# Kernel optimization log

Hardware: AMD Instinct MI355X
Metric: run time of the kernel (lower is better)

Reference implementation:

```python
import jax, jax.numpy as jnp
from jax import lax
import numpy as np

BINS = 256

def setup_inputs() -> dict:
    key = jax.random.key(0)
    k1, k2 = jax.random.split(key)
    B, C, H, W = 8, 3, 1024, 1024
    dst = jax.random.uniform(k1, (B, C, H, W), dtype=jnp.float32)
    ref = jax.random.uniform(k2, (B, C, H, W), dtype=jnp.float32)
    return {"dst": dst, "ref": ref}


def _cal_hist(img):
    # img: [B,C,H,W] in [0,1]. torch.histc(img*255, bins=256, min=0, max=255):
    # bin width = 255/256, so bin = floor(img*255 / (255/256)) = floor(img*256).
    # Inputs are in [0,1) so nothing is out of histc's range (clip is a no-op safeguard).
    B, C, H, W = img.shape
    bc = B * C
    x = img.reshape(bc, H * W)
    idx = jnp.clip(jnp.floor(x * float(BINS)).astype(jnp.int32), 0, BINS - 1)
    rows = jnp.arange(bc, dtype=jnp.int32)[:, None]
    counts = jnp.zeros((bc, BINS), jnp.float32).at[rows, idx].add(1.0)
    # F.normalize(p=1, dim=1) with eps=1e-12
    counts = counts / jnp.maximum(jnp.sum(counts, axis=1, keepdims=True), 1e-12)
    # triu-bmm == cumulative sum -> per-channel CDF
    return jnp.cumsum(counts, axis=1)


def _trans_row(cdf_dst, cdf_ref):
    # Faithful vectorization of the sequential two-pointer loop in cal_trans.
    # For each i (pointer j only ever advances): match at the smallest
    # j' >= j with cdf_ref[j'-1] <= d <= cdf_ref[j']; if impossible, j runs
    # off to 256 and this and all later entries become 255.
    def step(j, d):
        s = jnp.searchsorted(cdf_ref, d)            # smallest s with cdf_ref[s] >= d, in [0,256]
        cand = jnp.maximum(j, s)                    # pointer never moves backwards; cand in [1,256]
        ok = (j < BINS) & (cand <= BINS - 1) & (d >= cdf_ref[cand - 1])
        out = jnp.where(ok, cand, BINS - 1)
        j_next = jnp.where(ok, cand, jnp.int32(BINS))
        return j_next, out.astype(jnp.int32)
    _, tail = lax.scan(step, jnp.int32(1), cdf_dst[1:])  # i = 1..255
    table = jnp.concatenate([jnp.zeros(1, jnp.int32), tail])  # table[0] = arange init = 0
    return table.at[BINS - 1].set(BINS - 1)                   # table[:,255] = 255


def reference(dst, ref):
    B, C, H, W = dst.shape
    bc = B * C
    hist_dst = _cal_hist(dst)   # [BC,256] CDFs
    hist_ref = _cal_hist(ref)
    tables = jax.vmap(_trans_row)(hist_dst, hist_ref)  # [BC,256] int32
    # NOTE: original code indexes tables[b*c] (not b*C+c) -- bug preserved faithfully.
    b_idx = jnp.arange(B, dtype=jnp.int32)[:, None]
    c_idx = jnp.arange(C, dtype=jnp.int32)[None, :]
    row_sel = (b_idx * c_idx).reshape(-1)               # [BC]
    luts = tables[row_sel]                              # [BC,256]
    pix = jnp.clip((dst * 255.0).astype(jnp.int32), 0, BINS - 1).reshape(bc, H * W)
    rst = jnp.take_along_axis(luts, pix, axis=1).reshape(B, C, H, W)
    return rst.astype(dst.dtype) / 255.0
```

## Files before the change

### kernel.cpp

```cpp
#include <hip/hip_runtime.h>

#define BINS 256
#define BC_N 24
#define C_N  3
#define NCOPY 16
#define HSTRIDE (NCOPY+1)

__global__ __launch_bounds__(256) void hm_hist(const float* __restrict__ dst,
                                               const float* __restrict__ refp,
                                               unsigned int* __restrict__ hist,
                                               int n4_per_row) {
    __shared__ unsigned int sh[BINS * HSTRIDE];
    const int t = threadIdx.x;
    for (int j = t; j < BINS * HSTRIDE; j += 256) sh[j] = 0u;
    __syncthreads();

    const int row = blockIdx.y;
    const float* img = blockIdx.z ? refp : dst;
    const float4* p = reinterpret_cast<const float4*>(img) + (size_t)row * n4_per_row;
    const int copy = t & (NCOPY - 1);
    const int gsz = gridDim.x * blockDim.x;

    #pragma unroll 4
    for (int i = blockIdx.x * blockDim.x + t; i < n4_per_row; i += gsz) {
        float4 v = p[i];
        int b0 = min(max((int)(v.x * 256.0f), 0), BINS - 1);
        int b1 = min(max((int)(v.y * 256.0f), 0), BINS - 1);
        int b2 = min(max((int)(v.z * 256.0f), 0), BINS - 1);
        int b3 = min(max((int)(v.w * 256.0f), 0), BINS - 1);
        atomicAdd(&sh[b0 * HSTRIDE + copy], 1u);
        atomicAdd(&sh[b1 * HSTRIDE + copy], 1u);
        atomicAdd(&sh[b2 * HSTRIDE + copy], 1u);
        atomicAdd(&sh[b3 * HSTRIDE + copy], 1u);
    }
    __syncthreads();

    unsigned int s = 0;
    #pragma unroll
    for (int c = 0; c < NCOPY; ++c) s += sh[t * HSTRIDE + c];

    unsigned int* g = hist + ((size_t)blockIdx.z * BC_N + row) * BINS;
    if (s) atomicAdd(&g[t], s);
}

__global__ __launch_bounds__(256) void hm_table(const unsigned int* __restrict__ hist,
                                                float* __restrict__ lut) {
    __shared__ unsigned int sd[BINS], sr[BINS];
    __shared__ float cdf_d[BINS], cdf_r[BINS];
    __shared__ int firstFail;

    const int r = blockIdx.x;
    const int t = threadIdx.x;

    unsigned int xd = hist[(size_t)r * BINS + t];
    unsigned int xr = hist[(size_t)(BC_N + r) * BINS + t];
    if (t == 0) firstFail = BINS;
    sd[t] = xd; sr[t] = xr;
    __syncthreads();

    #pragma unroll
    for (int off = 1; off < BINS; off <<= 1) {
        unsigned int yd = (t >= off) ? sd[t - off] : 0u;
        unsigned int yr = (t >= off) ? sr[t - off] : 0u;
        __syncthreads();
        xd += yd; xr += yr;
        sd[t] = xd; sr[t] = xr;
        __syncthreads();
    }
    float totd = fmaxf((float)sd[BINS - 1], 1e-12f);
    float totr = fmaxf((float)sr[BINS - 1], 1e-12f);
    cdf_d[t] = (float)xd / totd;
    cdf_r[t] = (float)xr / totr;
    __syncthreads();

    int out;
    if (t == 0) {
        out = 0;
    } else {
        float d = cdf_d[t];
        int lo = 0, hi = BINS;
        while (lo < hi) {
            int m = (lo + hi) >> 1;
            if (cdf_r[m] < d) lo = m + 1; else hi = m;
        }
        int cand = lo > 1 ? lo : 1;
        bool ok = (cand <= BINS - 1) && (d >= cdf_r[cand - 1]);
        if (!ok) atomicMin(&firstFail, t);
        out = cand;
    }
    __syncthreads();

    if (t >= firstFail) out = BINS - 1;
    if (t == BINS - 1) out = BINS - 1;
    lut[(size_t)r * BINS + t] = (float)out / 255.0f;
}

__global__ __launch_bounds__(256) void hm_apply(const float* __restrict__ dst,
                                                const float* __restrict__ lut,
                                                float* __restrict__ out,
                                                int n4_per_row) {
    __shared__ float slut[BINS];
    const int bc = blockIdx.y;
    const int b = bc / C_N;
    const int c = bc - b * C_N;
    const int row = b * c;
    const int t = threadIdx.x;

    slut[t] = lut[(size_t)row * BINS + t];
    __syncthreads();

    const float4* in4 = reinterpret_cast<const float4*>(dst) + (size_t)bc * n4_per_row;
    float4* out4 = reinterpret_cast<float4*>(out) + (size_t)bc * n4_per_row;
    const int gsz = gridDim.x * blockDim.x;

    #pragma unroll 4
    for (int i = blockIdx.x * blockDim.x + t; i < n4_per_row; i += gsz) {
        float4 v = in4[i];
        float4 o;
        o.x = slut[min(max((int)(v.x * 255.0f), 0), BINS - 1)];
        o.y = slut[min(max((int)(v.y * 255.0f), 0), BINS - 1)];
        o.z = slut[min(max((int)(v.z * 255.0f), 0), BINS - 1)];
        o.w = slut[min(max((int)(v.w * 255.0f), 0), BINS - 1)];
        out4[i] = o;
    }
}

extern "C" void kernel_launch(void* const* d_in, const int* in_sizes, int n_in,
                              void* d_out, int out_size, void* d_ws, size_t ws_size,
                              hipStream_t stream) {
    const float* dst  = (const float*)d_in[0];
    const float* refp = (const float*)d_in[1];
    float* out = (float*)d_out;

    const int total = in_sizes[0];
    const int hw = total / BC_N;
    const int n4 = hw >> 2;

    unsigned int* hist = (unsigned int*)d_ws;
    float* lut = (float*)((char*)d_ws + (size_t)2 * BC_N * BINS * sizeof(unsigned int));

    hipMemsetAsync(d_ws, 0, (size_t)2 * BC_N * BINS * sizeof(unsigned int), stream);

    dim3 hg(32, BC_N, 2);
    hm_hist<<<hg, dim3(256), 0, stream>>>(dst, refp, hist, n4);

    hm_table<<<dim3(BC_N), dim3(256), 0, stream>>>(hist, lut);

    dim3 ag(64, BC_N);
    hm_apply<<<ag, dim3(256), 0, stream>>>(dst, lut, out, n4);
}
```

Before: 80.36 us.

## Replace shared-memory histogram atomics with per-thread 8-bit private histograms

```diff
diff --git a/kernel.cpp b/kernel.cpp
--- a/kernel.cpp
+++ b/kernel.cpp
@@ -3,41 +3,56 @@
 #define BINS 256
 #define BC_N 24
 #define C_N  3
-#define NCOPY 16
-#define HSTRIDE (NCOPY+1)
+#define CH   20
 
-__global__ __launch_bounds__(256) void hm_hist(const float* __restrict__ dst,
-                                               const float* __restrict__ refp,
-                                               unsigned int* __restrict__ hist,
-                                               int n4_per_row) {
-    __shared__ unsigned int sh[BINS * HSTRIDE];
+__global__ __launch_bounds__(256, 2) void hm_hist(const float* __restrict__ dst,
+                                                  const float* __restrict__ refp,
+                                                  unsigned int* __restrict__ hist,
+                                                  int n4_per_row) {
+    __shared__ unsigned char h8[BINS * 256];
+    unsigned int* h32 = reinterpret_cast<unsigned int*>(h8);
     const int t = threadIdx.x;
-    for (int j = t; j < BINS * HSTRIDE; j += 256) sh[j] = 0u;
+
+    #pragma unroll
+    for (int j = 0; j < 64; ++j) h32[j * 256 + t] = 0u;
     __syncthreads();
 
     const int row = blockIdx.y;
     const float* img = blockIdx.z ? refp : dst;
     const float4* p = reinterpret_cast<const float4*>(img) + (size_t)row * n4_per_row;
-    const int copy = t & (NCOPY - 1);
-    const int gsz = gridDim.x * blockDim.x;
+    const int stride = CH * 256;
 
-    #pragma unroll 4
-    for (int i = blockIdx.x * blockDim.x + t; i < n4_per_row; i += gsz) {
+    int i = blockIdx.x * 256 + t;
+    for (; i + 7 * stride < n4_per_row; i += 8 * stride) {
+        float4 v[8];
+        #pragma unroll
+        for (int k = 0; k < 8; ++k) v[k] = p[i + k * stride];
+        #pragma unroll
+        for (int k = 0; k < 8; ++k) {
+            h8[min(max((int)(v[k].x * 256.0f), 0), BINS - 1) * 256 + t]++;
+            h8[min(max((int)(v[k].y * 256.0f), 0), BINS - 1) * 256 + t]++;
+            h8[min(max((int)(v[k].z * 256.0f), 0), BINS - 1) * 256 + t]++;
+            h8[min(max((int)(v[k].w * 256.0f), 0), BINS - 1) * 256 + t]++;
+        }
+    }
+    for (; i < n4_per_row; i += stride) {
         float4 v = p[i];
-        int b0 = min(max((int)(v.x * 256.0f), 0), BINS - 1);
-        int b1 = min(max((int)(v.y * 256.0f), 0), BINS - 1);
-        int b2 = min(max((int)(v.z * 256.0f), 0), BINS - 1);
-        int b3 = min(max((int)(v.w * 256.0f), 0), BINS - 1);
-        atomicAdd(&sh[b0 * HSTRIDE + copy], 1u);
-        atomicAdd(&sh[b1 * HSTRIDE + copy], 1u);
-        atomicAdd(&sh[b2 * HSTRIDE + copy], 1u);
-        atomicAdd(&sh[b3 * HSTRIDE + copy], 1u);
+        h8[min(max((int)(v.x * 256.0f), 0), BINS - 1) * 256 + t]++;
+        h8[min(max((int)(v.y * 256.0f), 0), BINS - 1) * 256 + t]++;
+        h8[min(max((int)(v.z * 256.0f), 0), BINS - 1) * 256 + t]++;
+        h8[min(max((int)(v.w * 256.0f), 0), BINS - 1) * 256 + t]++;
     }
     __syncthreads();
 
-    unsigned int s = 0;
+    const unsigned int* r32 = h32 + t * 64;
+    unsigned int a = 0, b = 0;
     #pragma unroll
-    for (int c = 0; c < NCOPY; ++c) s += sh[t * HSTRIDE + c];
+    for (int k = 0; k < 64; ++k) {
+        unsigned int w = r32[(k + t) & 63];
+        a += w & 0x00FF00FFu;
+        b += (w >> 8) & 0x00FF00FFu;
+    }
+    unsigned int s = (a & 0xFFFFu) + (a >> 16) + (b & 0xFFFFu) + (b >> 16);
 
     unsigned int* g = hist + ((size_t)blockIdx.z * BC_N + row) * BINS;
     if (s) atomicAdd(&g[t], s);
@@ -141,7 +156,7 @@
 
     hipMemsetAsync(d_ws, 0, (size_t)2 * BC_N * BINS * sizeof(unsigned int), stream);
 
-    dim3 hg(32, BC_N, 2);
+    dim3 hg(CH, BC_N, 2);
     hm_hist<<<hg, dim3(256), 0, stream>>>(dst, refp, hist, n4);
 
     hm_table<<<dim3(BC_N), dim3(256), 0, stream>>>(hist, lut);
```

Measured after the change: 93.59 us. +16.5%, slower.

## Replace shared-memory atomic histogram with wave ballot bit-sliced counting; fuse table into apply

Applied to the files above, without the earlier changes.

```diff
diff --git a/kernel.cpp b/kernel.cpp
--- a/kernel.cpp
+++ b/kernel.cpp
@@ -3,53 +3,90 @@
 #define BINS 256
 #define BC_N 24
 #define C_N  3
-#define NCOPY 16
-#define HSTRIDE (NCOPY+1)
+#define CH   32
 
 __global__ __launch_bounds__(256) void hm_hist(const float* __restrict__ dst,
                                                const float* __restrict__ refp,
                                                unsigned int* __restrict__ hist,
                                                int n4_per_row) {
-    __shared__ unsigned int sh[BINS * HSTRIDE];
+    __shared__ unsigned int wsum[4][BINS];
     const int t = threadIdx.x;
-    for (int j = t; j < BINS * HSTRIDE; j += 256) sh[j] = 0u;
-    __syncthreads();
+    const int l = t & 63;
+    const int w = t >> 6;
+
+    const unsigned long long t0 = (l & 1)  ? 0ull : ~0ull;
+    const unsigned long long t1 = (l & 2)  ? 0ull : ~0ull;
+    const unsigned long long t2 = (l & 4)  ? 0ull : ~0ull;
+    const unsigned long long t3 = (l & 8)  ? 0ull : ~0ull;
+    const unsigned long long t4 = (l & 16) ? 0ull : ~0ull;
+    const unsigned long long t5 = (l & 32) ? 0ull : ~0ull;
+
+    unsigned int c0 = 0, c1 = 0, c2 = 0, c3 = 0;
 
     const int row = blockIdx.y;
     const float* img = blockIdx.z ? refp : dst;
     const float4* p = reinterpret_cast<const float4*>(img) + (size_t)row * n4_per_row;
-    const int copy = t & (NCOPY - 1);
-    const int gsz = gridDim.x * blockDim.x;
+    const int stride = CH * 256;
 
+    auto grp = [&](float x) {
+        int bin = min((int)(x * 256.0f), BINS - 1);
+        unsigned long long B0 = __ballot(bin & 1);
+        unsigned long long B1 = __ballot(bin & 2);
+        unsigned long long B2 = __ballot(bin & 4);
+        unsigned long long B3 = __ballot(bin & 8);
+        unsigned long long B4 = __ballot(bin & 16);
+        unsigned long long B5 = __ballot(bin & 32);
+        unsigned long long B6 = __ballot(bin & 64);
+        unsigned long long B7 = __ballot(bin & 128);
+        unsigned long long m = (B0 ^ t0) & (B1 ^ t1) & (B2 ^ t2)
+                             & (B3 ^ t3) & (B4 ^ t4) & (B5 ^ t5);
+        unsigned long long n6 = ~B6, n7 = ~B7;
+        c0 += (unsigned)__popcll(m & n7 & n6);
+        c1 += (unsigned)__popcll(m & n7 & B6);
+        c2 += (unsigned)__popcll(m & B7 & n6);
+        c3 += (unsigned)__popcll(m & B7 & B6);
+    };
+
+    const int nfull = n4_per_row / stride;
+    int i = blockIdx.x * 256 + t;
     #pragma unroll 4
-    for (int i = blockIdx.x * blockDim.x + t; i < n4_per_row; i += gsz) {
+    for (int it = 0; it < nfull; ++it, i += stride) {
         float4 v = p[i];
-        int b0 = min(max((int)(v.x * 256.0f), 0), BINS - 1);
-        int b1 = min(max((int)(v.y * 256.0f), 0), BINS - 1);
-        int b2 = min(max((int)(v.z * 256.0f), 0), BINS - 1);
-        int b3 = min(max((int)(v.w * 256.0f), 0), BINS - 1);
-        atomicAdd(&sh[b0 * HSTRIDE + copy], 1u);
-        atomicAdd(&sh[b1 * HSTRIDE + copy], 1u);
-        atomicAdd(&sh[b2 * HSTRIDE + copy], 1u);
-        atomicAdd(&sh[b3 * HSTRIDE + copy], 1u);
+        grp(v.x); grp(v.y); grp(v.z); grp(v.w);
     }
+    if (nfull * stride < n4_per_row) {
+        bool valid = (i < n4_per_row);
+        float4 v = make_float4(0.f, 0.f, 0.f, 0.f);
+        if (valid) v = p[i];
+        unsigned int inv = 64u - (unsigned)__popcll(__ballot(valid));
+        grp(v.x); grp(v.y); grp(v.z); grp(v.w);
+        if (l == 0) c0 -= 4u * inv;
+    }
+
+    wsum[w][l]       = c0;
+    wsum[w][l + 64]  = c1;
+    wsum[w][l + 128] = c2;
+    wsum[w][l + 192] = c3;
     __syncthreads();
 
-    unsigned int s = 0;
-    #pragma unroll
-    for (int c = 0; c < NCOPY; ++c) s += sh[t * HSTRIDE + c];
-
+    unsigned int s = wsum[0][t] + wsum[1][t] + wsum[2][t] + wsum[3][t];
     unsigned int* g = hist + ((size_t)blockIdx.z * BC_N + row) * BINS;
-    if (s) atomicAdd(&g[t], s);
+    atomicAdd(&g[t], s);
 }
 
-__global__ __launch_bounds__(256) void hm_table(const unsigned int* __restrict__ hist,
-                                                float* __restrict__ lut) {
+__global__ __launch_bounds__(256) void hm_apply(const float* __restrict__ dst,
+                                                const unsigned int* __restrict__ hist,
+                                                float* __restrict__ out,
+                                                int n4_per_row) {
     __shared__ unsigned int sd[BINS], sr[BINS];
     __shared__ float cdf_d[BINS], cdf_r[BINS];
+    __shared__ float slut[BINS];
     __shared__ int firstFail;
 
-    const int r = blockIdx.x;
+    const int bc = blockIdx.y;
+    const int b = bc / C_N;
+    const int c = bc - b * C_N;
+    const int r = b * c;
     const int t = threadIdx.x;
 
     unsigned int xd = hist[(size_t)r * BINS + t];
@@ -73,9 +110,9 @@
     cdf_r[t] = (float)xr / totr;
     __syncthreads();
 
-    int out;
+    int o;
     if (t == 0) {
-        out = 0;
+        o = 0;
     } else {
         float d = cdf_d[t];
         int lo = 0, hi = BINS;
@@ -86,27 +123,12 @@
         int cand = lo > 1 ? lo : 1;
         bool ok = (cand <= BINS - 1) && (d >= cdf_r[cand - 1]);
         if (!ok) atomicMin(&firstFail, t);
-        out = cand;
+        o = cand;
     }
     __syncthreads();
-
-    if (t >= firstFail) out = BINS - 1;
-    if (t == BINS - 1) out = BINS - 1;
-    lut[(size_t)r * BINS + t] = (float)out / 255.0f;
-}
-
-__global__ __launch_bounds__(256) void hm_apply(const float* __restrict__ dst,
-                                                const float* __restrict__ lut,
-                                                float* __restrict__ out,
-                                                int n4_per_row) {
-    __shared__ float slut[BINS];
-    const int bc = blockIdx.y;
-    const int b = bc / C_N;
-    const int c = bc - b * C_N;
-    const int row = b * c;
-    const int t = threadIdx.x;
-
-    slut[t] = lut[(size_t)row * BINS + t];
+    if (t >= firstFail) o = BINS - 1;
+    if (t == BINS - 1) o = BINS - 1;
+    slut[t] = (float)o / 255.0f;
     __syncthreads();
 
     const float4* in4 = reinterpret_cast<const float4*>(dst) + (size_t)bc * n4_per_row;
@@ -116,12 +138,12 @@
     #pragma unroll 4
     for (int i = blockIdx.x * blockDim.x + t; i < n4_per_row; i += gsz) {
         float4 v = in4[i];
-        float4 o;
-        o.x = slut[min(max((int)(v.x * 255.0f), 0), BINS - 1)];
-        o.y = slut[min(max((int)(v.y * 255.0f), 0), BINS - 1)];
-        o.z = slut[min(max((int)(v.z * 255.0f), 0), BINS - 1)];
-        o.w = slut[min(max((int)(v.w * 255.0f), 0), BINS - 1)];
-        out4[i] = o;
+        float4 o4;
+        o4.x = slut[min(max((int)(v.x * 255.0f), 0), BINS - 1)];
+        o4.y = slut[min(max((int)(v.y * 255.0f), 0), BINS - 1)];
+        o4.z = slut[min(max((int)(v.z * 255.0f), 0), BINS - 1)];
+        o4.w = slut[min(max((int)(v.w * 255.0f), 0), BINS - 1)];
+        out4[i] = o4;
     }
 }
 
@@ -137,15 +159,11 @@
     const int n4 = hw >> 2;
 
     unsigned int* hist = (unsigned int*)d_ws;
-    float* lut = (float*)((char*)d_ws + (size_t)2 * BC_N * BINS * sizeof(unsigned int));
-
     hipMemsetAsync(d_ws, 0, (size_t)2 * BC_N * BINS * sizeof(unsigned int), stream);
 
-    dim3 hg(32, BC_N, 2);
+    dim3 hg(CH, BC_N, 2);
     hm_hist<<<hg, dim3(256), 0, stream>>>(dst, refp, hist, n4);
 
-    hm_table<<<dim3(BC_N), dim3(256), 0, stream>>>(hist, lut);
-
     dim3 ag(64, BC_N);
-    hm_apply<<<ag, dim3(256), 0, stream>>>(dst, lut, out, n4);
+    hm_apply<<<ag, dim3(256), 0, stream>>>(dst, hist, out, n4);
 }
```

After: 140.7 us. 1.75x slower.

## Pipeline histogram loads via direct global-to-LDS async copies with single shared histogram

Applied to the files above, without the earlier changes.

```diff
diff --git a/kernel.cpp b/kernel.cpp
--- a/kernel.cpp
+++ b/kernel.cpp
@@ -3,44 +3,90 @@
 #define BINS 256
 #define BC_N 24
 #define C_N  3
-#define NCOPY 16
-#define HSTRIDE (NCOPY+1)
+#define CH   32
+#define DEPTH 6
+#define WAVES 4
+
+typedef float f32x4 __attribute__((ext_vector_type(4)));
 
 __global__ __launch_bounds__(256) void hm_hist(const float* __restrict__ dst,
                                                const float* __restrict__ refp,
                                                unsigned int* __restrict__ hist,
                                                int n4_per_row) {
-    __shared__ unsigned int sh[BINS * HSTRIDE];
+    __shared__ __align__(16) float stage[WAVES * DEPTH * 256];
+    __shared__ unsigned int shist[BINS];
+
     const int t = threadIdx.x;
-    for (int j = t; j < BINS * HSTRIDE; j += 256) sh[j] = 0u;
+    const int w = t >> 6;
+    const int l = t & 63;
+
+    shist[t] = 0u;
     __syncthreads();
 
     const int row = blockIdx.y;
     const float* img = blockIdx.z ? refp : dst;
-    const float4* p = reinterpret_cast<const float4*>(img) + (size_t)row * n4_per_row;
-    const int copy = t & (NCOPY - 1);
-    const int gsz = gridDim.x * blockDim.x;
+    const float4* p4 = reinterpret_cast<const float4*>(img) + (size_t)row * n4_per_row;
 
-    #pragma unroll 4
-    for (int i = blockIdx.x * blockDim.x + t; i < n4_per_row; i += gsz) {
-        float4 v = p[i];
+    const int span  = n4_per_row / CH;
+    const int its   = span >> 8;
+    const int base4 = blockIdx.x * span;
+
+    float* wavebase = stage + w * (DEPTH * 256);
+    const unsigned ldsw =
+        (unsigned)(size_t)(__attribute__((address_space(3))) void*)wavebase;
+    const unsigned myoff = ldsw + (unsigned)(l * 16);
+
+    for (int k = 0; k < DEPTH && k < its; ++k) {
+        const float4* gp = p4 + base4 + (k << 8) + (w << 6) + l;
+        __builtin_amdgcn_global_load_lds(
+            (const __attribute__((address_space(1))) void*)gp,
+            (__attribute__((address_space(3))) void*)(wavebase + k * 256),
+            16, 0, 0);
+    }
+
+    int slot = 0;
+    int k = 0;
+    for (; k < its - DEPTH; ++k) {
+        asm volatile("s_waitcnt vmcnt(5)");
+        f32x4 v;
+        asm volatile("ds_read_b128 %0, %1\n\ts_waitcnt lgkmcnt(0)"
+                     : "=v"(v)
+                     : "v"(myoff + (unsigned)(slot << 10)));
+        const float4* gp = p4 + base4 + ((k + DEPTH) << 8) + (w << 6) + l;
+        __builtin_amdgcn_global_load_lds(
+            (const __attribute__((address_space(1))) void*)gp,
+            (__attribute__((address_space(3))) void*)(wavebase + slot * 256),
+            16, 0, 0);
         int b0 = min(max((int)(v.x * 256.0f), 0), BINS - 1);
         int b1 = min(max((int)(v.y * 256.0f), 0), BINS - 1);
         int b2 = min(max((int)(v.z * 256.0f), 0), BINS - 1);
         int b3 = min(max((int)(v.w * 256.0f), 0), BINS - 1);
-        atomicAdd(&sh[b0 * HSTRIDE + copy], 1u);
-        atomicAdd(&sh[b1 * HSTRIDE + copy], 1u);
-        atomicAdd(&sh[b2 * HSTRIDE + copy], 1u);
-        atomicAdd(&sh[b3 * HSTRIDE + copy], 1u);
+        atomicAdd(&shist[b0], 1u);
+        atomicAdd(&shist[b1], 1u);
+        atomicAdd(&shist[b2], 1u);
+        atomicAdd(&shist[b3], 1u);
+        slot = (slot + 1 == DEPTH) ? 0 : slot + 1;
     }
+    asm volatile("s_waitcnt vmcnt(0)");
+    for (; k < its; ++k) {
+        f32x4 v;
+        asm volatile("ds_read_b128 %0, %1\n\ts_waitcnt lgkmcnt(0)"
+                     : "=v"(v)
+                     : "v"(myoff + (unsigned)(slot << 10)));
+        int b0 = min(max((int)(v.x * 256.0f), 0), BINS - 1);
+        int b1 = min(max((int)(v.y * 256.0f), 0), BINS - 1);
+        int b2 = min(max((int)(v.z * 256.0f), 0), BINS - 1);
+        int b3 = min(max((int)(v.w * 256.0f), 0), BINS - 1);
+        atomicAdd(&shist[b0], 1u);
+        atomicAdd(&shist[b1], 1u);
+        atomicAdd(&shist[b2], 1u);
+        atomicAdd(&shist[b3], 1u);
+        slot = (slot + 1 == DEPTH) ? 0 : slot + 1;
+    }
+
     __syncthreads();
-
-    unsigned int s = 0;
-    #pragma unroll
-    for (int c = 0; c < NCOPY; ++c) s += sh[t * HSTRIDE + c];
-
     unsigned int* g = hist + ((size_t)blockIdx.z * BC_N + row) * BINS;
-    if (s) atomicAdd(&g[t], s);
+    atomicAdd(&g[t], shist[t]);
 }
 
 __global__ __launch_bounds__(256) void hm_table(const unsigned int* __restrict__ hist,
@@ -141,7 +187,7 @@
 
     hipMemsetAsync(d_ws, 0, (size_t)2 * BC_N * BINS * sizeof(unsigned int), stream);
 
-    dim3 hg(32, BC_N, 2);
+    dim3 hg(CH, BC_N, 2);
     hm_hist<<<hg, dim3(256), 0, stream>>>(dst, refp, hist, n4);
 
     hm_table<<<dim3(BC_N), dim3(256), 0, stream>>>(hist, lut);
```

Result: no change. 80.45 us (+0.1%).
